# Kernel tuning notes

Measured on AMD Instinct MI355X. Metric: run time of the kernel, lower is better.

The kernel has to match this reference:

```python
import jax, jax.numpy as jnp
import numpy as np

EPS = 1e-5
NPOINT, RADIUS, NSAMPLE, HEADS, DH = 512, 0.2, 64, 8, 64


def _ln(x, g, b):
    m = jnp.mean(x, -1, keepdims=True)
    v = jnp.var(x, -1, keepdims=True)
    return (x - m) * jax.lax.rsqrt(v + EPS) * g + b


def _gather(points, idx):
    # points [B,N,C], idx [B,...] -> [B,...,C]
    b = jnp.arange(points.shape[0]).reshape((-1,) + (1,) * (idx.ndim - 1))
    return points[b, idx]


def _fps(xyz, npoint):
    # farthest point sampling, deterministic start at index 0
    B, N, _ = xyz.shape

    def step(carry, _):
        dist, far = carry
        cen = jnp.take_along_axis(xyz, far[:, None, None], axis=1)  # [B,1,3]
        d = jnp.sum((xyz - cen) ** 2, -1)  # [B,N]
        dist = jnp.minimum(dist, d)
        nxt = jnp.argmax(dist, -1).astype(jnp.int32)
        return (dist, nxt), far

    init = (jnp.full((B, N), 1e10, xyz.dtype), jnp.zeros((B,), jnp.int32))
    _, idxs = jax.lax.scan(step, init, None, length=npoint)
    return idxs.T  # [B,npoint]


def _ball_query(xyz, new_xyz):
    # xyz [B,N,3], new_xyz [B,S,3] -> idx [B,S,NSAMPLE]
    N = xyz.shape[1]
    sq = (jnp.sum(new_xyz ** 2, -1)[:, :, None] + jnp.sum(xyz ** 2, -1)[:, None, :]
          - 2.0 * jnp.einsum('bsc,bnc->bsn', new_xyz, xyz))  # [B,S,N]
    gidx = jnp.broadcast_to(jnp.arange(N), sq.shape)
    gidx = jnp.where(sq > RADIUS ** 2, N, gidx)
    neg, _ = jax.lax.top_k(-gidx, NSAMPLE)  # smallest NSAMPLE valid indices
    idx = -neg
    return jnp.where(idx == N, idx[:, :, :1], idx)


def reference(features, sa_w0, sa_b0, sa_w1, sa_b1, sa_w2, sa_b2,
              bn_g0, bn_b0, bn_m0, bn_v0, bn_g1, bn_b1, bn_m1, bn_v1,
              bn_g2, bn_b2, bn_m2, bn_v2,
              lift_w, lift_b, lift_g, lift_beta, cls_token,
              qkv_w, out_w, out_b, ln1_g, ln1_b,
              pe_w1, pe_b1, pe_w2, pe_b2, ln2_g, ln2_b,
              ff_w1, ff_b1, ff_w2, ff_b2):
    B = features.shape[0]
    dim = cls_token.shape[0]
    xyz = jnp.transpose(features, (0, 2, 1))  # [B,N,3] (in_dim=3 so points==xyz)
    pts = xyz

    # ---- PointNet set abstraction ----
    fps_idx = _fps(xyz, NPOINT)
    new_xyz = _gather(xyz, fps_idx)  # [B,S,3]
    idx = _ball_query(xyz, new_xyz)  # [B,S,K]
    g_xyz = _gather(xyz, idx)  # [B,S,K,3]
    g_norm = g_xyz - new_xyz[:, :, None, :]
    g_pts = _gather(pts, idx)
    h = jnp.concatenate([g_norm, g_pts], -1)  # [B,S,K,6]
    h = jnp.transpose(h, (0, 3, 2, 1))  # [B,C,K,S]
    for (w, bb, g, be, m, v) in ((sa_w0, sa_b0, bn_g0, bn_b0, bn_m0, bn_v0),
                                 (sa_w1, sa_b1, bn_g1, bn_b1, bn_m1, bn_v1),
                                 (sa_w2, sa_b2, bn_g2, bn_b2, bn_m2, bn_v2)):
        h = jnp.einsum('bcks,oc->boks', h, w) + bb[None, :, None, None]
        h = (h - m[None, :, None, None]) * jax.lax.rsqrt(v[None, :, None, None] + EPS) \
            * g[None, :, None, None] + be[None, :, None, None]
        h = jax.nn.relu(h)
    feat = jnp.max(h, axis=2)  # [B,sa_dim,S]
    cent = jnp.transpose(new_xyz, (0, 2, 1))  # [B,3,S]

    # ---- lift ----
    x = jnp.einsum('bcs,oc->bos', jnp.concatenate([cent, feat], 1), lift_w) + lift_b[None, :, None]
    x = jnp.transpose(x, (0, 2, 1))  # [B,S,dim]
    x = _ln(x, lift_g, lift_beta)

    # ---- cls token + centroid deltas ----
    x = jnp.concatenate([jnp.broadcast_to(cls_token, (B, 1, dim)), x], 1)  # [B,n,dim]
    cent = jnp.concatenate([jnp.zeros((B, 3, 1), x.dtype), cent], -1)  # [B,3,n]
    delta = cent[:, :, :, None] - cent[:, :, None, :]  # [B,3,n,n]

    # ---- transformer ----
    scale = DH ** -0.5
    depth = qkv_w.shape[0]
    n = x.shape[1]
    for l in range(depth):
        h1 = _ln(x, ln1_g[l], ln1_b[l])
        qkv = h1 @ qkv_w[l]  # [B,n,3*inner]
        q, k, v = jnp.split(qkv, 3, -1)
        q = q.reshape(B, n, HEADS, DH).transpose(0, 2, 1, 3)
        k = k.reshape(B, n, HEADS, DH).transpose(0, 2, 1, 3)
        v = v.reshape(B, n, HEADS, DH).transpose(0, 2, 1, 3)
        pe = jax.nn.relu(jnp.einsum('bcij,oc->boij', delta, pe_w1[l]) + pe_b1[l][None, :, None, None])
        pe = jnp.einsum('bcij,oc->boij', pe, pe_w2[l]) + pe_b2[l][None, :, None, None]  # [B,1,n,n]
        dots = (jnp.einsum('bhid,bhjd->bhij', q, k) + pe) * scale
        attn = jax.nn.softmax(dots, -1)
        o = jnp.einsum('bhij,bhjd->bhid', attn, v).transpose(0, 2, 1, 3).reshape(B, n, HEADS * DH)
        x = x + (o @ out_w[l] + out_b[l])
        h2 = _ln(x, ln2_g[l], ln2_b[l])
        x = x + (jax.nn.gelu(h2 @ ff_w1[l] + ff_b1[l], approximate=False) @ ff_w2[l] + ff_b2[l])
    return x[:, 0]


def setup_inputs() -> dict:
    key = jax.random.key(0)
    ks = iter(jax.random.split(key, 64))

    def rnd(shape, s=0.02):
        return (jax.random.normal(next(ks), shape, jnp.float32) * s)

    D, dim, inner, mlp, sad = 6, 512, 512, 1024, 256
    inp = {}
    inp['features'] = jax.random.uniform(next(ks), (2, 3, 10000), jnp.float32, -1.0, 1.0)
    inp['sa_w0'] = rnd((64, 6), 0.2); inp['sa_b0'] = jnp.zeros((64,), jnp.float32)
    inp['sa_w1'] = rnd((64, 64), 0.1); inp['sa_b1'] = jnp.zeros((64,), jnp.float32)
    inp['sa_w2'] = rnd((sad, 64), 0.1); inp['sa_b2'] = jnp.zeros((sad,), jnp.float32)
    for i, c in ((0, 64), (1, 64), (2, sad)):
        inp[f'bn_g{i}'] = jnp.ones((c,), jnp.float32)
        inp[f'bn_b{i}'] = jnp.zeros((c,), jnp.float32)
        inp[f'bn_m{i}'] = jnp.zeros((c,), jnp.float32)
        inp[f'bn_v{i}'] = jnp.ones((c,), jnp.float32)
    inp['lift_w'] = rnd((dim, sad + 3), 0.05)
    inp['lift_b'] = jnp.zeros((dim,), jnp.float32)
    inp['lift_g'] = jnp.ones((dim,), jnp.float32)
    inp['lift_beta'] = jnp.zeros((dim,), jnp.float32)
    inp['cls_token'] = rnd((dim,), 1.0)
    inp['qkv_w'] = rnd((D, dim, 3 * inner))
    inp['out_w'] = rnd((D, inner, dim))
    inp['out_b'] = jnp.zeros((D, dim), jnp.float32)
    inp['ln1_g'] = jnp.ones((D, dim), jnp.float32)
    inp['ln1_b'] = jnp.zeros((D, dim), jnp.float32)
    inp['pe_w1'] = rnd((D, 64, 3), 0.1)
    inp['pe_b1'] = jnp.zeros((D, 64), jnp.float32)
    inp['pe_w2'] = rnd((D, 1, 64), 0.1)
    inp['pe_b2'] = jnp.zeros((D, 1), jnp.float32)
    inp['ln2_g'] = jnp.ones((D, dim), jnp.float32)
    inp['ln2_b'] = jnp.zeros((D, dim), jnp.float32)
    inp['ff_w1'] = rnd((D, dim, mlp))
    inp['ff_b1'] = jnp.zeros((D, mlp), jnp.float32)
    inp['ff_w2'] = rnd((D, mlp, dim))
    inp['ff_b2'] = jnp.zeros((D, dim), jnp.float32)
    return inp
```

## Files before the change

### kernel.cpp

```cpp
#include <hip/hip_runtime.h>
#include <math.h>

#define NPTS 10000
#define NP   512
#define NS   64
#define NTOK 513
#define DIM  512
#define NHEADS 8
#define DH   64
#define DEPTH 6
#define SAD  256
#define MLPD 1024
#define EPSV 1e-5f

typedef float  f32x2  __attribute__((ext_vector_type(2)));
typedef float  f32x4  __attribute__((ext_vector_type(4)));
typedef __bf16 bf16x8 __attribute__((ext_vector_type(8)));
typedef unsigned short u16x4 __attribute__((ext_vector_type(4)));
typedef unsigned short u16x8 __attribute__((ext_vector_type(8)));

__device__ __forceinline__ unsigned short f2bf(float x) {
    unsigned u = __float_as_uint(x);
    unsigned r = u + 0x7fffu + ((u >> 16) & 1u);
    return (unsigned short)(r >> 16);
}
__device__ __forceinline__ bf16x8 bf8_from_f32(const float* p) {
    u16x8 h;
    #pragma unroll
    for (int e = 0; e < 8; e++) h[e] = f2bf(p[e]);
    return *(bf16x8*)&h;
}

__device__ __forceinline__ float blk_sum256(float v, float* red) {
    #pragma unroll
    for (int off = 32; off; off >>= 1) v += __shfl_down(v, off);
    __syncthreads();
    if ((threadIdx.x & 63) == 0) red[threadIdx.x >> 6] = v;
    __syncthreads();
    return red[0] + red[1] + red[2] + red[3];
}

__global__ __launch_bounds__(256) void fps_wconv_kernel(
        const float* __restrict__ f, float* __restrict__ cent3,
        const float* __restrict__ qkv_w, unsigned short* __restrict__ qkvT,
        const float* __restrict__ out_w, unsigned short* __restrict__ outT,
        const float* __restrict__ ff_w1, unsigned short* __restrict__ ff1T,
        const float* __restrict__ ff_w2, unsigned short* __restrict__ ff2T) {
    #pragma clang fp contract(off)
    __shared__ unsigned long long spk[2][4];
    __shared__ float scx[2][4], scy[2][4], scz[2][4];
    __shared__ unsigned short tl[64][65];

    if (blockIdx.x >= 2) {
        int id = blockIdx.x - 2;
        const float* Ws; unsigned short* Wd; int K, N, tn, per;
        if (id < 1152)      { Ws = qkv_w; Wd = qkvT; K = 512;  N = 1536; tn = 24; per = 192; }
        else if (id < 1536) { id -= 1152; Ws = out_w; Wd = outT; K = 512; N = 512; tn = 8;  per = 64;  }
        else if (id < 2304) { id -= 1536; Ws = ff_w1; Wd = ff1T; K = 512; N = 1024; tn = 16; per = 128; }
        else                { id -= 2304; Ws = ff_w2; Wd = ff2T; K = 1024; N = 512; tn = 8;  per = 128; }
        const int l = id / per, rem = id % per;
        const int n0 = (rem % tn) * 64, k0 = (rem / tn) * 64;
        Ws += (size_t)l * K * N;
        Wd += (size_t)l * K * N;
        const int ty = threadIdx.x >> 4, c4 = (threadIdx.x & 15) * 4;
        #pragma unroll
        for (int i = 0; i < 4; i++) {
            int r = ty + 16 * i;
            f32x4 v = *(const f32x4*)(Ws + (size_t)(k0 + r) * N + n0 + c4);
            tl[c4 + 0][r] = f2bf(v.x);
            tl[c4 + 1][r] = f2bf(v.y);
            tl[c4 + 2][r] = f2bf(v.z);
            tl[c4 + 3][r] = f2bf(v.w);
        }
        __syncthreads();
        #pragma unroll
        for (int i = 0; i < 4; i++) {
            int r = ty + 16 * i;
            u16x4 hv = { tl[r][c4], tl[r][c4 + 1], tl[r][c4 + 2], tl[r][c4 + 3] };
            *(u16x4*)(Wd + (size_t)(n0 + r) * K + k0 + c4) = hv;
        }
        return;
    }

    const int b = blockIdx.x;
    const float* fx = f + (size_t)b * 3 * NPTS;
    const float* fy = fx + NPTS;
    const float* fz = fx + 2 * NPTS;
    const int t = threadIdx.x;
    const int wv = t >> 6, lane = t & 63;

    f32x2 px[20], py[20], pz[20], dist[20];
    #pragma unroll
    for (int q = 0; q < 20; q++) {
        #pragma unroll
        for (int e = 0; e < 2; e++) {
            int p = t + (2 * q + e) * 256;
            if (p < NPTS) { px[q][e] = fx[p]; py[q][e] = fy[p]; pz[q][e] = fz[p]; dist[q][e] = 1e10f; }
            else          { px[q][e] = 0.f;  py[q][e] = 0.f;  pz[q][e] = 0.f;  dist[q][e] = -1.0f; }
        }
    }
    if (t == 0) {
        float* c0 = cent3 + (size_t)b * NTOK * 3;
        c0[0] = 0.f; c0[1] = 0.f; c0[2] = 0.f;
    }
    float cx = fx[0], cy = fy[0], cz = fz[0];

    for (int it = 0; it < NP; ++it) {
        if (t == 0) {
            float* c = cent3 + (size_t)(b * NTOK + 1 + it) * 3;
            c[0] = cx; c[1] = cy; c[2] = cz;
        }
        const f32x2 c2x = {cx, cx}, c2y = {cy, cy}, c2z = {cz, cz};
        float bv = -1.0f; unsigned bi = 0xffffffffu;
        #pragma unroll
        for (int q = 0; q < 20; q++) {
            f32x2 dx = px[q] - c2x;
            f32x2 dy = py[q] - c2y;
            f32x2 dz = pz[q] - c2z;
            f32x2 s1 = dx * dx;
            f32x2 s2 = dy * dy;
            f32x2 s3 = dz * dz;
            f32x2 d  = (s1 + s2) + s3;
            f32x2 nd = __builtin_elementwise_min(dist[q], d);
            dist[q] = nd;
            if (nd.x > bv) { bv = nd.x; bi = t + (2 * q) * 256; }
            if (nd.y > bv) { bv = nd.y; bi = t + (2 * q + 1) * 256; }
        }
        unsigned long long best = ((unsigned long long)__float_as_uint(bv) << 32)
                                | (unsigned long long)(~bi);
        #pragma unroll
        for (int off = 32; off; off >>= 1) {
            unsigned long long o = __shfl_down(best, off);
            best = (o > best) ? o : best;
        }
        int wis = __builtin_amdgcn_readfirstlane((int)(~(unsigned)best));
        float wx = fx[wis], wy = fy[wis], wz = fz[wis];
        const int cur = it & 1;
        if (lane == 0) {
            spk[cur][wv] = best;
            scx[cur][wv] = wx; scy[cur][wv] = wy; scz[cur][wv] = wz;
        }
        __syncthreads();
        unsigned long long g = spk[cur][0]; int bw = 0;
        #pragma unroll
        for (int w = 1; w < 4; w++) {
            unsigned long long o = spk[cur][w];
            if (o > g) { g = o; bw = w; }
        }
        cx = scx[cur][bw]; cy = scy[cur][bw]; cz = scz[cur][bw];
    }
}

__global__ __launch_bounds__(256) void ballmlp_kernel(
        const float* __restrict__ f, const float* __restrict__ cent3,
        const float* __restrict__ w0, const float* __restrict__ b0,
        const float* __restrict__ g0, const float* __restrict__ be0,
        const float* __restrict__ m0, const float* __restrict__ v0,
        const float* __restrict__ w1, const float* __restrict__ b1,
        const float* __restrict__ g1, const float* __restrict__ be1,
        const float* __restrict__ m1, const float* __restrict__ v1,
        const float* __restrict__ w2, const float* __restrict__ b2,
        const float* __restrict__ g2, const float* __restrict__ be2,
        const float* __restrict__ m2, const float* __restrict__ v2,
        float* __restrict__ featb) {
    const int bs = blockIdx.x;
    const int b = bs / NP, s = bs % NP;
    const int tid = threadIdx.x;
    const int wv = tid >> 6, lane = tid & 63;
    const int fr = lane & 15, fq = lane >> 4;

    __shared__ int sidx[NS];
    __shared__ alignas(16) unsigned short Xl[64][8];
    __shared__ alignas(16) unsigned short H1[64][72];
    __shared__ alignas(16) unsigned short H2[64][72];

    const float* fx = f + (size_t)b * 3 * NPTS;
    const float* fy = fx + NPTS;
    const float* fz = fx + 2 * NPTS;
    const float* c  = cent3 + (size_t)(b * NTOK + 1 + s) * 3;
    const float nx = c[0], ny = c[1], nz = c[2];

    const int c1 = 16 * wv + fr;
    const float sc0 = g0[c1] / sqrtf(v0[c1] + EPSV);
    const float off0 = (b0[c1] - m0[c1]) * sc0 + be0[c1];
    const float sc1 = g1[c1] / sqrtf(v1[c1] + EPSV);
    const float off1 = (b1[c1] - m1[c1]) * sc1 + be1[c1];

    u16x8 b0h = {0,0,0,0,0,0,0,0};
    if (fq == 0) {
        const float* wr = w0 + c1 * 6;
        #pragma unroll
        for (int e = 0; e < 6; e++) b0h[e] = f2bf(wr[e]);
    }
    bf16x8 bf0 = *(bf16x8*)&b0h;
    bf16x8 bf1[2];
    #pragma unroll
    for (int ks = 0; ks < 2; ks++)
        bf1[ks] = bf8_from_f32(w1 + (size_t)c1 * 64 + ks * 32 + fq * 8);

    if (wv == 0) {
        const float nn = __fadd_rn(__fadd_rn(__fmul_rn(nx, nx), __fmul_rn(ny, ny)), __fmul_rn(nz, nz));
        int cnt = 0, first = -1;
        for (int base = 0; base < NPTS; base += 64) {
            const int p = base + lane;
            bool valid = false;
            if (p < NPTS) {
                float x = fx[p], y = fy[p], z = fz[p];
                float pp = __fadd_rn(__fadd_rn(__fmul_rn(x, x), __fmul_rn(y, y)), __fmul_rn(z, z));
                float dt = __fadd_rn(__fadd_rn(__fmul_rn(nx, x), __fmul_rn(ny, y)), __fmul_rn(nz, z));
                float sq = __fsub_rn(__fadd_rn(nn, pp), __fmul_rn(2.0f, dt));
                valid = !(sq > 0.04f);
            }
            unsigned long long m = __ballot(valid);
            if (first < 0 && m) first = base + __builtin_ctzll(m);
            int pos = cnt + __popcll(m & ((1ull << lane) - 1ull));
            if (valid && pos < NS) sidx[pos] = p;
            cnt += __popcll(m);
            if (cnt >= NS) break;
        }
        for (int pos = cnt + lane; pos < NS; pos += 64) sidx[pos] = first;
    }
    __syncthreads();

    if (tid < 64) {
        const int p = sidx[tid];
        float i3 = fx[p], i4 = fy[p], i5 = fz[p];
        u16x8 xv;
        xv[0] = f2bf(i3 - nx); xv[1] = f2bf(i4 - ny); xv[2] = f2bf(i5 - nz);
        xv[3] = f2bf(i3); xv[4] = f2bf(i4); xv[5] = f2bf(i5);
        xv[6] = 0; xv[7] = 0;
        *(u16x8*)(&Xl[tid][0]) = xv;
    }
    __syncthreads();

    const u16x8 z8 = {0,0,0,0,0,0,0,0};
    const bf16x8 zf = *(const bf16x8*)&z8;

    #pragma unroll
    for (int m = 0; m < 4; m++) {
        bf16x8 af = (fq == 0) ? *(const bf16x8*)(&Xl[m * 16 + fr][0]) : zf;
        f32x4 d = (f32x4){0.f, 0.f, 0.f, 0.f};
        d = __builtin_amdgcn_mfma_f32_16x16x32_bf16(af, bf0, d, 0, 0, 0);
        #pragma unroll
        for (int j = 0; j < 4; j++) {
            float v = fmaxf(d[j] * sc0 + off0, 0.f);
            H1[m * 16 + fq * 4 + j][16 * wv + fr] = f2bf(v);
        }
    }
    __syncthreads();

    #pragma unroll
    for (int m = 0; m < 4; m++) {
        f32x4 d = (f32x4){0.f, 0.f, 0.f, 0.f};
        #pragma unroll
        for (int ks = 0; ks < 2; ks++) {
            bf16x8 af = *(const bf16x8*)(&H1[m * 16 + fr][ks * 32 + fq * 8]);
            d = __builtin_amdgcn_mfma_f32_16x16x32_bf16(af, bf1[ks], d, 0, 0, 0);
        }
        #pragma unroll
        for (int j = 0; j < 4; j++) {
            float v = fmaxf(d[j] * sc1 + off1, 0.f);
            H2[m * 16 + fq * 4 + j][16 * wv + fr] = f2bf(v);
        }
    }
    __syncthreads();

    bf16x8 af2[4][2];
    #pragma unroll
    for (int m = 0; m < 4; m++)
        #pragma unroll
        for (int ks = 0; ks < 2; ks++)
            af2[m][ks] = *(const bf16x8*)(&H2[m * 16 + fr][ks * 32 + fq * 8]);

    float* outp = featb + (size_t)bs * SAD;
    #pragma unroll
    for (int t = 0; t < 4; t++) {
        const int c2 = 64 * wv + 16 * t + fr;
        const float sc2 = g2[c2] / sqrtf(v2[c2] + EPSV);
        const float off2 = (b2[c2] - m2[c2]) * sc2 + be2[c2];
        bf16x8 bf2[2];
        #pragma unroll
        for (int ks = 0; ks < 2; ks++)
            bf2[ks] = bf8_from_f32(w2 + (size_t)c2 * 64 + ks * 32 + fq * 8);
        float mx = -INFINITY;
        #pragma unroll
        for (int m = 0; m < 4; m++) {
            f32x4 d = (f32x4){0.f, 0.f, 0.f, 0.f};
            d = __builtin_amdgcn_mfma_f32_16x16x32_bf16(af2[m][0], bf2[0], d, 0, 0, 0);
            d = __builtin_amdgcn_mfma_f32_16x16x32_bf16(af2[m][1], bf2[1], d, 0, 0, 0);
            #pragma unroll
            for (int j = 0; j < 4; j++)
                mx = fmaxf(mx, fmaxf(d[j] * sc2 + off2, 0.f));
        }
        mx = fmaxf(mx, __shfl_xor(mx, 16));
        mx = fmaxf(mx, __shfl_xor(mx, 32));
        if (fq == 0) outp[c2] = mx;
    }
}

__global__ __launch_bounds__(256) void lift_ln_kernel(const float* __restrict__ cent3,
                                                      const float* __restrict__ featb,
                                                      const float* __restrict__ lw,
                                                      const float* __restrict__ lb,
                                                      const float* __restrict__ lg,
                                                      const float* __restrict__ lbeta,
                                                      const float* __restrict__ cls,
                                                      float* __restrict__ x) {
    const int t = threadIdx.x;
    if (blockIdx.x < 2) {
        int b = blockIdx.x;
        x[(size_t)(b * NTOK) * DIM + t]       = cls[t];
        x[(size_t)(b * NTOK) * DIM + t + 256] = cls[t + 256];
        return;
    }
    const int bs = blockIdx.x - 2;
    const int b = bs / NP, s = bs % NP;
    __shared__ float si[259];
    __shared__ float sy[512];
    __shared__ float red[4];
    if (t < 3) si[t] = cent3[(size_t)(b * NTOK + 1 + s) * 3 + t];
    si[3 + t] = featb[(size_t)bs * SAD + t];
    __syncthreads();
    for (int o = t; o < DIM; o += 256) {
        const float* wr = lw + (size_t)o * 259;
        float acc = lb[o];
        for (int ci = 0; ci < 259; ci++) acc += wr[ci] * si[ci];
        sy[o] = acc;
    }
    __syncthreads();
    float tot  = blk_sum256(sy[t] + sy[t + 256], red);
    float mean = tot * (1.0f / 512.0f);
    float d0 = sy[t] - mean, d1 = sy[t + 256] - mean;
    float var = blk_sum256(d0 * d0 + d1 * d1, red) * (1.0f / 512.0f);
    float inv = 1.0f / sqrtf(var + EPSV);
    float* xr = x + (size_t)(b * NTOK + 1 + s) * DIM;
    xr[t]       = d0 * inv * lg[t]       + lbeta[t];
    xr[t + 256] = d1 * inv * lg[t + 256] + lbeta[t + 256];
}

__global__ __launch_bounds__(256) void ln_kernel(const float* __restrict__ xin,
                                                 const float* __restrict__ g,
                                                 const float* __restrict__ beta,
                                                 unsigned short* __restrict__ y) {
    const int r = blockIdx.x;
    const float* xr = xin + (size_t)r * DIM;
    const int t = threadIdx.x;
    float a0 = xr[t], a1 = xr[t + 256];
    __shared__ float red[4];
    float mean = blk_sum256(a0 + a1, red) * (1.0f / 512.0f);
    float d0 = a0 - mean, d1 = a1 - mean;
    float var = blk_sum256(d0 * d0 + d1 * d1, red) * (1.0f / 512.0f);
    float inv = 1.0f / sqrtf(var + EPSV);
    unsigned short* yr = y + (size_t)r * DIM;
    yr[t]       = f2bf(d0 * inv * g[t]       + beta[t]);
    yr[t + 256] = f2bf(d1 * inv * g[t + 256] + beta[t + 256]);
}

__global__ __launch_bounds__(256) void pe_all_kernel(const float* __restrict__ cent3,
                                                     const float* __restrict__ pw1_,
                                                     const float* __restrict__ pb1_,
                                                     const float* __restrict__ pw2_,
                                                     const float* __restrict__ pb2_,
                                                     float* __restrict__ pebuf) {
    const int l = blockIdx.y;
    const float* pw1 = pw1_ + l * 192;
    const float* pb1 = pb1_ + l * 64;
    const float* pw2 = pw2_ + l * 64;
    long gid = (long)blockIdx.x * 256 + threadIdx.x;
    const long total = 2L * NTOK * NTOK;
    if (gid >= total) return;
    int j = (int)(gid % NTOK);
    long r = gid / NTOK;
    int i = (int)(r % NTOK);
    int b = (int)(r / NTOK);
    const float* ci = cent3 + (size_t)(b * NTOK + i) * 3;
    const float* cj = cent3 + (size_t)(b * NTOK + j) * 3;
    float d0 = ci[0] - cj[0], d1 = ci[1] - cj[1], d2 = ci[2] - cj[2];
    float acc = pb2_[l];
    #pragma unroll 8
    for (int c = 0; c < 64; c++) {
        float tv = pw1[c * 3] * d0 + pw1[c * 3 + 1] * d1 + pw1[c * 3 + 2] * d2 + pb1[c];
        acc += pw2[c] * fmaxf(tv, 0.f);
    }
    pebuf[(size_t)l * total + gid] = acc;
}

__global__ __launch_bounds__(256) void attn_mfma_kernel(const unsigned short* __restrict__ qkv,
                                                        const float* __restrict__ pebuf,
                                                        unsigned short* __restrict__ obuf) {
    __shared__ alignas(16) unsigned short Qs[64][72];
    __shared__ alignas(16) unsigned short Ks[64][72];
    __shared__ alignas(16) unsigned short Vt[64][72];
    __shared__ alignas(16) unsigned short Ps[64][72];

    const int ti = blockIdx.x;
    const int bh = blockIdx.y;
    const int b = bh >> 3, h = bh & 7;
    const int i0 = ti * 64;
    const int tid = threadIdx.x;
    const int w = tid >> 6, lane = tid & 63;
    const int fr = lane & 15, fq = lane >> 4;
    const int fko = fq * 8;

    const unsigned short* qbase = qkv + (size_t)b * NTOK * (3 * DIM) + h * DH;
    const int sr = tid >> 2, sc = (tid & 3) * 16;

    {
        int i = i0 + sr;
        u16x8 v0 = {0,0,0,0,0,0,0,0}, v1 = {0,0,0,0,0,0,0,0};
        if (i < NTOK) {
            v0 = *(const u16x8*)(qbase + (size_t)i * (3 * DIM) + sc);
            v1 = *(const u16x8*)(qbase + (size_t)i * (3 * DIM) + sc + 8);
        }
        *(u16x8*)(&Qs[sr][sc]) = v0;
        *(u16x8*)(&Qs[sr][sc + 8]) = v1;
    }

    float mrow[4], lrow[4];
    f32x4 od[4];
    #pragma unroll
    for (int r = 0; r < 4; r++) { mrow[r] = -INFINITY; lrow[r] = 0.f; }
    #pragma unroll
    for (int dt = 0; dt < 4; dt++) od[dt] = (f32x4){0.f, 0.f, 0.f, 0.f};

    const unsigned short* kbase = qkv + (size_t)b * NTOK * (3 * DIM) + DIM + h * DH;
    const unsigned short* vbase = qkv + (size_t)b * NTOK * (3 * DIM) + 2 * DIM + h * DH;

    for (int jc = 0; jc < 9; jc++) {
        const int j0 = jc * 64;
        const int wj = (NTOK - j0) < 64 ? (NTOK - j0) : 64;
        __syncthreads();
        if (sr < wj) {
            const unsigned short* kp = kbase + (size_t)(j0 + sr) * (3 * DIM) + sc;
            const unsigned short* vp = vbase + (size_t)(j0 + sr) * (3 * DIM) + sc;
            u16x8 k0 = *(const u16x8*)(kp);
            u16x8 k1 = *(const u16x8*)(kp + 8);
            *(u16x8*)(&Ks[sr][sc]) = k0;
            *(u16x8*)(&Ks[sr][sc + 8]) = k1;
            u16x8 q0 = *(const u16x8*)(vp);
            u16x8 q1 = *(const u16x8*)(vp + 8);
            #pragma unroll
            for (int e = 0; e < 8; e++) {
                Vt[sc + e][sr] = q0[e];
                Vt[sc + 8 + e][sr] = q1[e];
            }
        } else {
            u16x8 z = {0,0,0,0,0,0,0,0};
            *(u16x8*)(&Ks[sr][sc]) = z;
            *(u16x8*)(&Ks[sr][sc + 8]) = z;
            #pragma unroll
            for (int e = 0; e < 16; e++) Vt[sc + e][sr] = 0;
        }
        __syncthreads();

        bf16x8 qf0 = *(const bf16x8*)(&Qs[16 * w + fr][fko]);
        bf16x8 qf1 = *(const bf16x8*)(&Qs[16 * w + fr][fko + 32]);
        f32x4 sa[4];
        #pragma unroll
        for (int jt = 0; jt < 4; jt++) {
            f32x4 acc = (f32x4){0.f, 0.f, 0.f, 0.f};
            bf16x8 kf0 = *(const bf16x8*)(&Ks[jt * 16 + fr][fko]);
            bf16x8 kf1 = *(const bf16x8*)(&Ks[jt * 16 + fr][fko + 32]);
            acc = __builtin_amdgcn_mfma_f32_16x16x32_bf16(qf0, kf0, acc, 0, 0, 0);
            acc = __builtin_amdgcn_mfma_f32_16x16x32_bf16(qf1, kf1, acc, 0, 0, 0);
            sa[jt] = acc;
        }

        float sv[4][4];
        float cm[4] = {-INFINITY, -INFINITY, -INFINITY, -INFINITY};
        #pragma unroll
        for (int jt = 0; jt < 4; jt++) {
            int jl = jt * 16 + fr;
            int jg = j0 + jl; if (jg > NTOK - 1) jg = NTOK - 1;
            #pragma unroll
            for (int r = 0; r < 4; r++) {
                int i = i0 + 16 * w + fq * 4 + r; if (i > NTOK - 1) i = NTOK - 1;
                float pe = pebuf[((size_t)b * NTOK + i) * NTOK + jg];
                float s = (sa[jt][r] + pe) * 0.125f;
                s = (jl < wj) ? s : -INFINITY;
                sv[jt][r] = s;
                cm[r] = fmaxf(cm[r], s);
            }
        }
        #pragma unroll
        for (int off = 1; off < 16; off <<= 1) {
            #pragma unroll
            for (int r = 0; r < 4; r++) cm[r] = fmaxf(cm[r], __shfl_xor(cm[r], off));
        }
        float fac[4], rs[4];
        #pragma unroll
        for (int r = 0; r < 4; r++) {
            float mn = fmaxf(mrow[r], cm[r]);
            fac[r] = __expf(mrow[r] - mn);
            mrow[r] = mn;
            rs[r] = 0.f;
        }
        #pragma unroll
        for (int jt = 0; jt < 4; jt++) {
            #pragma unroll
            for (int r = 0; r < 4; r++) {
                float p = __expf(sv[jt][r] - mrow[r]);
                rs[r] += p;
                Ps[16 * w + fq * 4 + r][jt * 16 + fr] = f2bf(p);
            }
        }
        #pragma unroll
        for (int off = 1; off < 16; off <<= 1) {
            #pragma unroll
            for (int r = 0; r < 4; r++) rs[r] += __shfl_xor(rs[r], off);
        }
        #pragma unroll
        for (int r = 0; r < 4; r++) lrow[r] = lrow[r] * fac[r] + rs[r];
        #pragma unroll
        for (int dt = 0; dt < 4; dt++) {
            #pragma unroll
            for (int r = 0; r < 4; r++) od[dt][r] *= fac[r];
        }

        bf16x8 pf0 = *(const bf16x8*)(&Ps[16 * w + fr][fko]);
        bf16x8 pf1 = *(const bf16x8*)(&Ps[16 * w + fr][fko + 32]);
        #pragma unroll
        for (int dt = 0; dt < 4; dt++) {
            bf16x8 vf0 = *(const bf16x8*)(&Vt[dt * 16 + fr][fko]);
            bf16x8 vf1 = *(const bf16x8*)(&Vt[dt * 16 + fr][fko + 32]);
            od[dt] = __builtin_amdgcn_mfma_f32_16x16x32_bf16(pf0, vf0, od[dt], 0, 0, 0);
            od[dt] = __builtin_amdgcn_mfma_f32_16x16x32_bf16(pf1, vf1, od[dt], 0, 0, 0);
        }
    }

    #pragma unroll
    for (int r = 0; r < 4; r++) {
        int i = i0 + 16 * w + fq * 4 + r;
        if (i >= NTOK) continue;
        float inv = 1.0f / lrow[r];
        #pragma unroll
        for (int dt = 0; dt < 4; dt++) {
            obuf[((size_t)b * NTOK + i) * DIM + h * DH + dt * 16 + fr] = f2bf(od[dt][r] * inv);
        }
    }
}

template <int BM, int BN, int ACT, int OBF>
__global__ __launch_bounds__(256) void gemm_bt_kernel(const unsigned short* __restrict__ A,
                                                      const unsigned short* __restrict__ Bt,
                                                      const float* __restrict__ bias,
                                                      const float* __restrict__ resid,
                                                      void* __restrict__ Cv,
                                                      int M, int N, int K) {
    constexpr int FM = BM / 32, FN = BN / 32;
    __shared__ unsigned short Al[BM][72];
    __shared__ unsigned short Bl[BN][72];
    const int tid = threadIdx.x;
    const int bm = blockIdx.y * BM, bn = blockIdx.x * BN;
    const int wid = tid >> 6, lane = tid & 63;
    const int wr = (wid >> 1) * (BM / 2), wc = (wid & 1) * (BN / 2);
    const int fr = lane & 15, fko = (lane >> 4) * 8;
    const int srow = tid >> 3, sc8 = (tid & 7) * 8;

    f32x4 acc[FM][FN];
    #pragma unroll
    for (int m = 0; m < FM; m++)
        #pragma unroll
        for (int n = 0; n < FN; n++) acc[m][n] = (f32x4){0.f, 0.f, 0.f, 0.f};

    for (int kt = 0; kt < K; kt += 64) {
        #pragma unroll
        for (int q = 0; q < BM / 32; q++) {
            int r = srow + q * 32;
            int row = bm + r;
            u16x8 va = {0,0,0,0,0,0,0,0};
            if (row < M) va = *(const u16x8*)(A + (size_t)row * K + kt + sc8);
            *(u16x8*)(&Al[r][sc8]) = va;
        }
        #pragma unroll
        for (int q = 0; q < BN / 32; q++) {
            int r = srow + q * 32;
            u16x8 vb = *(const u16x8*)(Bt + (size_t)(bn + r) * K + kt + sc8);
            *(u16x8*)(&Bl[r][sc8]) = vb;
        }
        __syncthreads();
        #pragma unroll
        for (int ks = 0; ks < 2; ks++) {
            bf16x8 af[FM], bfr[FN];
            #pragma unroll
            for (int m = 0; m < FM; m++) af[m]  = *(const bf16x8*)(&Al[wr + m * 16 + fr][ks * 32 + fko]);
            #pragma unroll
            for (int n = 0; n < FN; n++) bfr[n] = *(const bf16x8*)(&Bl[wc + n * 16 + fr][ks * 32 + fko]);
            #pragma unroll
            for (int m = 0; m < FM; m++)
                #pragma unroll
                for (int n = 0; n < FN; n++)
                    acc[m][n] = __builtin_amdgcn_mfma_f32_16x16x32_bf16(af[m], bfr[n], acc[m][n], 0, 0, 0);
        }
        __syncthreads();
    }

    float* Cf = (float*)Cv;
    unsigned short* Cb = (unsigned short*)Cv;
    const int rg = (lane >> 4) * 4;
    #pragma unroll
    for (int m = 0; m < FM; m++) {
        #pragma unroll
        for (int n = 0; n < FN; n++) {
            int col = bn + wc + n * 16 + fr;
            float bv = bias ? bias[col] : 0.f;
            #pragma unroll
            for (int j = 0; j < 4; j++) {
                int row = bm + wr + m * 16 + rg + j;
                if (row >= M) continue;
                float v = acc[m][n][j] + bv;
                if (ACT == 1) v = 0.5f * v * (1.0f + erff(v * 0.70710678118654752f));
                if (resid) v += resid[(size_t)row * N + col];
                if (OBF) Cb[(size_t)row * N + col] = f2bf(v);
                else     Cf[(size_t)row * N + col] = v;
            }
        }
    }
}

__global__ void copyout_kernel(const float* __restrict__ x, float* __restrict__ out) {
    int t = blockIdx.x * 256 + threadIdx.x;
    if (t < 2 * DIM) {
        int b = t >> 9, d = t & 511;
        out[t] = x[(size_t)(b * NTOK) * DIM + d];
    }
}

extern "C" void kernel_launch(void* const* d_in, const int* in_sizes, int n_in,
                              void* d_out, int out_size, void* d_ws, size_t ws_size,
                              hipStream_t stream) {
    const float* f      = (const float*)d_in[0];
    const float* sa_w0  = (const float*)d_in[1];
    const float* sa_b0  = (const float*)d_in[2];
    const float* sa_w1  = (const float*)d_in[3];
    const float* sa_b1  = (const float*)d_in[4];
    const float* sa_w2  = (const float*)d_in[5];
    const float* sa_b2  = (const float*)d_in[6];
    const float* bn_g0  = (const float*)d_in[7];
    const float* bn_b0  = (const float*)d_in[8];
    const float* bn_m0  = (const float*)d_in[9];
    const float* bn_v0  = (const float*)d_in[10];
    const float* bn_g1  = (const float*)d_in[11];
    const float* bn_b1  = (const float*)d_in[12];
    const float* bn_m1  = (const float*)d_in[13];
    const float* bn_v1  = (const float*)d_in[14];
    const float* bn_g2  = (const float*)d_in[15];
    const float* bn_b2  = (const float*)d_in[16];
    const float* bn_m2  = (const float*)d_in[17];
    const float* bn_v2  = (const float*)d_in[18];
    const float* lift_w = (const float*)d_in[19];
    const float* lift_b = (const float*)d_in[20];
    const float* lift_g = (const float*)d_in[21];
    const float* lift_be= (const float*)d_in[22];
    const float* cls    = (const float*)d_in[23];
    const float* qkv_w  = (const float*)d_in[24];
    const float* out_w  = (const float*)d_in[25];
    const float* out_b  = (const float*)d_in[26];
    const float* ln1_g  = (const float*)d_in[27];
    const float* ln1_b  = (const float*)d_in[28];
    const float* pe_w1  = (const float*)d_in[29];
    const float* pe_b1  = (const float*)d_in[30];
    const float* pe_w2  = (const float*)d_in[31];
    const float* pe_b2  = (const float*)d_in[32];
    const float* ln2_g  = (const float*)d_in[33];
    const float* ln2_b  = (const float*)d_in[34];
    const float* ff_w1  = (const float*)d_in[35];
    const float* ff_b1  = (const float*)d_in[36];
    const float* ff_w2  = (const float*)d_in[37];
    const float* ff_b2  = (const float*)d_in[38];

    char* ws = (char*)d_ws;
    size_t off = 0;
    auto alloc = [&](size_t bytes) -> char* {
        char* p = ws + off;
        off = (off + bytes + 255) & ~(size_t)255;
        return p;
    };
    float* cent3 = (float*)alloc((size_t)2 * NTOK * 3 * 4);
    float* featb = (float*)alloc((size_t)2 * NP * SAD * 4);
    float* xbuf  = (float*)alloc((size_t)2 * NTOK * DIM * 4);
    unsigned short* h1buf = (unsigned short*)alloc((size_t)2 * NTOK * DIM * 2);
    unsigned short* qkvb  = (unsigned short*)alloc((size_t)2 * NTOK * 3 * DIM * 2);
    unsigned short* obuf  = (unsigned short*)alloc((size_t)2 * NTOK * DIM * 2);
    unsigned short* hff   = (unsigned short*)alloc((size_t)2 * NTOK * MLPD * 2);
    float* pebuf = (float*)alloc((size_t)DEPTH * 2 * NTOK * NTOK * 4);
    unsigned short* qkvT = (unsigned short*)alloc((size_t)DEPTH * 3 * DIM * DIM * 2);
    unsigned short* outT = (unsigned short*)alloc((size_t)DEPTH * DIM * DIM * 2);
    unsigned short* ff1T = (unsigned short*)alloc((size_t)DEPTH * DIM * MLPD * 2);
    unsigned short* ff2T = (unsigned short*)alloc((size_t)DEPTH * MLPD * DIM * 2);

    fps_wconv_kernel<<<3074, 256, 0, stream>>>(f, cent3,
        qkv_w, qkvT, out_w, outT, ff_w1, ff1T, ff_w2, ff2T);
    ballmlp_kernel<<<2 * NP, 256, 0, stream>>>(f, cent3,
        sa_w0, sa_b0, bn_g0, bn_b0, bn_m0, bn_v0,
        sa_w1, sa_b1, bn_g1, bn_b1, bn_m1, bn_v1,
        sa_w2, sa_b2, bn_g2, bn_b2, bn_m2, bn_v2, featb);
    lift_ln_kernel<<<2 * NP + 2, 256, 0, stream>>>(cent3, featb, lift_w, lift_b, lift_g, lift_be, cls, xbuf);
    {
        long total = 2L * NTOK * NTOK;
        int blocks = (int)((total + 255) / 256);
        pe_all_kernel<<<dim3(blocks, 6), 256, 0, stream>>>(cent3, pe_w1, pe_b1, pe_w2, pe_b2, pebuf);
    }

    const int M = 2 * NTOK;
    const int GY = (M + 63) / 64;
    const size_t peL = 2L * NTOK * NTOK;
    for (int l = 0; l < DEPTH; l++) {
        ln_kernel<<<M, 256, 0, stream>>>(xbuf, ln1_g + l * DIM, ln1_b + l * DIM, h1buf);
        gemm_bt_kernel<64, 64, 0, 1><<<dim3(24, GY), 256, 0, stream>>>(
            h1buf, qkvT + (size_t)l * 3 * DIM * DIM, nullptr, nullptr, qkvb, M, 3 * DIM, DIM);
        attn_mfma_kernel<<<dim3(9, 16), 256, 0, stream>>>(qkvb, pebuf + (size_t)l * peL, obuf);
        gemm_bt_kernel<64, 32, 0, 0><<<dim3(16, GY), 256, 0, stream>>>(
            obuf, outT + (size_t)l * DIM * DIM, out_b + l * DIM, xbuf, xbuf, M, DIM, DIM);
        ln_kernel<<<M, 256, 0, stream>>>(xbuf, ln2_g + l * DIM, ln2_b + l * DIM, h1buf);
        gemm_bt_kernel<64, 64, 1, 1><<<dim3(16, GY), 256, 0, stream>>>(
            h1buf, ff1T + (size_t)l * DIM * MLPD, ff_b1 + l * MLPD, nullptr, hff, M, MLPD, DIM);
        gemm_bt_kernel<64, 32, 0, 0><<<dim3(16, GY), 256, 0, stream>>>(
            hff, ff2T + (size_t)l * MLPD * DIM, ff_b2 + l * DIM, xbuf, xbuf, M, DIM, MLPD);
    }
    copyout_kernel<<<4, 256, 0, stream>>>(xbuf, (float*)d_out);
}
```

Baseline: 1.444 ms.

## Simplify FPS argmax reduction and fuse positional-encoding into ball-query MLP kernel

The FPS loop drops the 64-bit packed value/index reduction in favour of a float-only max reduction. A second pass then finds the smallest matching index, but only in waves that hold the global max. This shortens the per-iteration serial critical path of the single-block FPS. Separately, the positional-encoding precompute blocks are appended to the ball-query MLP launch, saving one kernel launch and letting both workloads fill the GPU together. The cost is an extra __syncthreads per FPS iteration and a larger heterogeneous grid.

```diff
diff --git a/kernel.cpp b/kernel.cpp
--- a/kernel.cpp
+++ b/kernel.cpp
@@ -12,6 +12,7 @@
 #define SAD  256
 #define MLPD 1024
 #define EPSV 1e-5f
+#define PEB  2057
 
 typedef float  f32x2  __attribute__((ext_vector_type(2)));
 typedef float  f32x4  __attribute__((ext_vector_type(4)));
@@ -47,8 +48,8 @@
         const float* __restrict__ ff_w1, unsigned short* __restrict__ ff1T,
         const float* __restrict__ ff_w2, unsigned short* __restrict__ ff2T) {
     #pragma clang fp contract(off)
-    __shared__ unsigned long long spk[2][4];
-    __shared__ float scx[2][4], scy[2][4], scz[2][4];
+    __shared__ float swv[2][4];
+    __shared__ unsigned scand[2][4];
     __shared__ unsigned short tl[64][65];
 
     if (blockIdx.x >= 2) {
@@ -111,7 +112,7 @@
             c[0] = cx; c[1] = cy; c[2] = cz;
         }
         const f32x2 c2x = {cx, cx}, c2y = {cy, cy}, c2z = {cz, cz};
-        float bv = -1.0f; unsigned bi = 0xffffffffu;
+        f32x2 mx2 = {-1.0f, -1.0f};
         #pragma unroll
         for (int q = 0; q < 20; q++) {
             f32x2 dx = px[q] - c2x;
@@ -123,35 +124,44 @@
             f32x2 d  = (s1 + s2) + s3;
             f32x2 nd = __builtin_elementwise_min(dist[q], d);
             dist[q] = nd;
-            if (nd.x > bv) { bv = nd.x; bi = t + (2 * q) * 256; }
-            if (nd.y > bv) { bv = nd.y; bi = t + (2 * q + 1) * 256; }
-        }
-        unsigned long long best = ((unsigned long long)__float_as_uint(bv) << 32)
-                                | (unsigned long long)(~bi);
-        #pragma unroll
-        for (int off = 32; off; off >>= 1) {
-            unsigned long long o = __shfl_down(best, off);
-            best = (o > best) ? o : best;
-        }
-        int wis = __builtin_amdgcn_readfirstlane((int)(~(unsigned)best));
-        float wx = fx[wis], wy = fy[wis], wz = fz[wis];
+            mx2 = __builtin_elementwise_max(mx2, nd);
+        }
+        const float tb = fmaxf(mx2.x, mx2.y);
+        float wb = tb;
+        #pragma unroll
+        for (int off = 1; off < 64; off <<= 1) wb = fmaxf(wb, __shfl_xor(wb, off));
         const int cur = it & 1;
-        if (lane == 0) {
-            spk[cur][wv] = best;
-            scx[cur][wv] = wx; scy[cur][wv] = wy; scz[cur][wv] = wz;
-        }
+        if (lane == 0) swv[cur][wv] = wb;
         __syncthreads();
-        unsigned long long g = spk[cur][0]; int bw = 0;
-        #pragma unroll
-        for (int w = 1; w < 4; w++) {
-            unsigned long long o = spk[cur][w];
-            if (o > g) { g = o; bw = w; }
-        }
-        cx = scx[cur][bw]; cy = scy[cur][bw]; cz = scz[cur][bw];
-    }
-}
-
-__global__ __launch_bounds__(256) void ballmlp_kernel(
+        const float gmax = fmaxf(fmaxf(swv[cur][0], swv[cur][1]),
+                                 fmaxf(swv[cur][2], swv[cur][3]));
+        unsigned cand = 0xffffffffu;
+        if (wb == gmax) {
+            if (tb == gmax) {
+                #pragma unroll
+                for (int q = 19; q >= 0; q--) {
+                    if (dist[q][1] == gmax) cand = (unsigned)((2 * q + 1) * 256 + t);
+                    if (dist[q][0] == gmax) cand = (unsigned)((2 * q) * 256 + t);
+                }
+            }
+            #pragma unroll
+            for (int off = 1; off < 64; off <<= 1) {
+                unsigned o = __shfl_xor(cand, off);
+                cand = (o < cand) ? o : cand;
+            }
+        }
+        if (lane == 0) scand[cur][wv] = cand;
+        __syncthreads();
+        unsigned widx = scand[cur][0];
+        widx = scand[cur][1] < widx ? scand[cur][1] : widx;
+        widx = scand[cur][2] < widx ? scand[cur][2] : widx;
+        widx = scand[cur][3] < widx ? scand[cur][3] : widx;
+        widx = (unsigned)__builtin_amdgcn_readfirstlane((int)widx);
+        cx = fx[widx]; cy = fy[widx]; cz = fz[widx];
+    }
+}
+
+__global__ __launch_bounds__(256) void ballmlp_pe_kernel(
         const float* __restrict__ f, const float* __restrict__ cent3,
         const float* __restrict__ w0, const float* __restrict__ b0,
         const float* __restrict__ g0, const float* __restrict__ be0,
@@ -162,7 +172,36 @@
         const float* __restrict__ w2, const float* __restrict__ b2,
         const float* __restrict__ g2, const float* __restrict__ be2,
         const float* __restrict__ m2, const float* __restrict__ v2,
-        float* __restrict__ featb) {
+        float* __restrict__ featb,
+        const float* __restrict__ pw1_, const float* __restrict__ pb1_,
+        const float* __restrict__ pw2_, const float* __restrict__ pb2_,
+        float* __restrict__ pebuf) {
+    if (blockIdx.x >= 2 * NP) {
+        const int id = blockIdx.x - 2 * NP;
+        const int l = id / PEB, rem = id % PEB;
+        const float* pw1 = pw1_ + l * 192;
+        const float* pb1 = pb1_ + l * 64;
+        const float* pw2 = pw2_ + l * 64;
+        const long total = 2L * NTOK * NTOK;
+        long gid = (long)rem * 256 + threadIdx.x;
+        if (gid >= total) return;
+        int j = (int)(gid % NTOK);
+        long r = gid / NTOK;
+        int i = (int)(r % NTOK);
+        int b = (int)(r / NTOK);
+        const float* ci = cent3 + (size_t)(b * NTOK + i) * 3;
+        const float* cj = cent3 + (size_t)(b * NTOK + j) * 3;
+        float d0 = ci[0] - cj[0], d1 = ci[1] - cj[1], d2 = ci[2] - cj[2];
+        float acc = pb2_[l];
+        #pragma unroll 8
+        for (int c = 0; c < 64; c++) {
+            float tv = pw1[c * 3] * d0 + pw1[c * 3 + 1] * d1 + pw1[c * 3 + 2] * d2 + pb1[c];
+            acc += pw2[c] * fmaxf(tv, 0.f);
+        }
+        pebuf[(size_t)l * total + gid] = acc;
+        return;
+    }
+
     const int bs = blockIdx.x;
     const int b = bs / NP, s = bs % NP;
     const int tid = threadIdx.x;
@@ -354,35 +393,6 @@
     unsigned short* yr = y + (size_t)r * DIM;
     yr[t]       = f2bf(d0 * inv * g[t]       + beta[t]);
     yr[t + 256] = f2bf(d1 * inv * g[t + 256] + beta[t + 256]);
-}
-
-__global__ __launch_bounds__(256) void pe_all_kernel(const float* __restrict__ cent3,
-                                                     const float* __restrict__ pw1_,
-                                                     const float* __restrict__ pb1_,
-                                                     const float* __restrict__ pw2_,
-                                                     const float* __restrict__ pb2_,
-                                                     float* __restrict__ pebuf) {
-    const int l = blockIdx.y;
-    const float* pw1 = pw1_ + l * 192;
-    const float* pb1 = pb1_ + l * 64;
-    const float* pw2 = pw2_ + l * 64;
-    long gid = (long)blockIdx.x * 256 + threadIdx.x;
-    const long total = 2L * NTOK * NTOK;
-    if (gid >= total) return;
-    int j = (int)(gid % NTOK);
-    long r = gid / NTOK;
-    int i = (int)(r % NTOK);
-    int b = (int)(r / NTOK);
-    const float* ci = cent3 + (size_t)(b * NTOK + i) * 3;
-    const float* cj = cent3 + (size_t)(b * NTOK + j) * 3;
-    float d0 = ci[0] - cj[0], d1 = ci[1] - cj[1], d2 = ci[2] - cj[2];
-    float acc = pb2_[l];
-    #pragma unroll 8
-    for (int c = 0; c < 64; c++) {
-        float tv = pw1[c * 3] * d0 + pw1[c * 3 + 1] * d1 + pw1[c * 3 + 2] * d2 + pb1[c];
-        acc += pw2[c] * fmaxf(tv, 0.f);
-    }
-    pebuf[(size_t)l * total + gid] = acc;
 }
 
 __global__ __launch_bounds__(256) void attn_mfma_kernel(const unsigned short* __restrict__ qkv,
@@ -691,16 +701,12 @@
 
     fps_wconv_kernel<<<3074, 256, 0, stream>>>(f, cent3,
         qkv_w, qkvT, out_w, outT, ff_w1, ff1T, ff_w2, ff2T);
-    ballmlp_kernel<<<2 * NP, 256, 0, stream>>>(f, cent3,
+    ballmlp_pe_kernel<<<2 * NP + DEPTH * PEB, 256, 0, stream>>>(f, cent3,
         sa_w0, sa_b0, bn_g0, bn_b0, bn_m0, bn_v0,
         sa_w1, sa_b1, bn_g1, bn_b1, bn_m1, bn_v1,
-        sa_w2, sa_b2, bn_g2, bn_b2, bn_m2, bn_v2, featb);
+        sa_w2, sa_b2, bn_g2, bn_b2, bn_m2, bn_v2, featb,
+        pe_w1, pe_b1, pe_w2, pe_b2, pebuf);
     lift_ln_kernel<<<2 * NP + 2, 256, 0, stream>>>(cent3, featb, lift_w, lift_b, lift_g, lift_be, cls, xbuf);
-    {
-        long total = 2L * NTOK * NTOK;
-        int blocks = (int)((total + 255) / 256);
-        pe_all_kernel<<<dim3(blocks, 6), 256, 0, stream>>>(cent3, pe_w1, pe_b1, pe_w2, pe_b2, pebuf);
-    }
 
     const int M = 2 * NTOK;
     const int GY = (M + 63) / 64;
```

After: 1.602 ms. 1.11x slower.
